# Performance work log

Hardware: AMD Instinct MI355X
Metric: run time of the kernel (lower is better)

Reference implementation:

```python
import jax, jax.numpy as jnp
import numpy as np

N_NODES = 10000


def gcn_conv(x, W, b, src, dst, num_nodes):
    # PyG GCNConv (eval): h = x @ W; add self-loops; symmetric norm D^-1/2 A D^-1/2; sum-aggregate; + bias
    h = x @ W  # [N, out]
    loop = jnp.arange(num_nodes, dtype=src.dtype)
    s = jnp.concatenate([src, loop])  # [E+N]
    d = jnp.concatenate([dst, loop])
    deg = jax.ops.segment_sum(jnp.ones_like(d, dtype=h.dtype), d, num_segments=num_nodes)
    dinv = jnp.where(deg > 0, jax.lax.rsqrt(deg), 0.0)
    norm = dinv[s] * dinv[d]  # [E+N]
    msg = h[s] * norm[:, None]  # gather + scale
    out = jax.ops.segment_sum(msg, d, num_segments=num_nodes)  # scatter-add to dst
    return out + b


def setup_inputs() -> dict:
    key = jax.random.key(0)
    k1, k2, k3, k4 = jax.random.split(key, 4)
    in_c, hid_c, out_c = 512, 512, 256
    x = jax.random.normal(k1, (N_NODES, in_c), dtype=jnp.float32)
    edge_index = jax.random.randint(k2, (2, 160000), 0, N_NODES, dtype=jnp.int64)
    W1 = jax.random.normal(k3, (in_c, hid_c), dtype=jnp.float32) * (1.0 / np.sqrt(in_c))
    b1 = jnp.zeros((hid_c,), dtype=jnp.float32)
    W2 = jax.random.normal(k4, (hid_c, out_c), dtype=jnp.float32) * (1.0 / np.sqrt(hid_c))
    b2 = jnp.zeros((out_c,), dtype=jnp.float32)
    return {"x": x, "edge_index": edge_index, "W1": W1, "b1": b1, "W2": W2, "b2": b2}


def reference(x, edge_index, W1, b1, W2, b2):
    src, dst = edge_index[0], edge_index[1]
    h = gcn_conv(x, W1, b1, src, dst, N_NODES)
    h = jax.nn.relu(h)
    # dropout(p=0.5) is identity in eval mode
    z = gcn_conv(h, W2, b2, src, dst, N_NODES)
    return z
```

## Files before the change

### kernel.cpp

```cpp
#include <hip/hip_runtime.h>

#define NN   10000

typedef float f32x4 __attribute__((ext_vector_type(4)));
typedef short s16x8 __attribute__((ext_vector_type(8)));
typedef short s16x4 __attribute__((ext_vector_type(4)));

__device__ __forceinline__ unsigned int f2bf(float f) {
  unsigned int u = __float_as_uint(f);
  return (u + 0x7fffu + ((u >> 16) & 1u)) >> 16;
}
__device__ __forceinline__ float bf2f(unsigned int h) {
  return __uint_as_float(h << 16);
}

__global__ void k_zero_int(int* __restrict__ p, int n) {
  int i = blockIdx.x * blockDim.x + threadIdx.x;
  if (i < n) p[i] = 0;
}

__global__ void k_count(const int* __restrict__ dst, int E, int* __restrict__ cnt) {
  int i = blockIdx.x * blockDim.x + threadIdx.x;
  if (i < E) atomicAdd(&cnt[dst[i]], 1);
}

__global__ __launch_bounds__(256) void k_scan(const int* __restrict__ cnt, int n,
                                              int* __restrict__ offs, float* __restrict__ dinv) {
  __shared__ int part[256];
  int t = threadIdx.x;
  int chunk = (n + 255) / 256;
  int lo = t * chunk, hi = min(lo + chunk, n);
  int s = 0;
  for (int i = lo; i < hi; ++i) s += cnt[i];
  part[t] = s;
  __syncthreads();
  for (int d = 1; d < 256; d <<= 1) {
    int v = (t >= d) ? part[t - d] : 0;
    __syncthreads();
    part[t] += v;
    __syncthreads();
  }
  int run = (t == 0) ? 0 : part[t - 1];
  for (int i = lo; i < hi; ++i) {
    offs[i] = run;
    int c = cnt[i];
    run += c;
    dinv[i] = rsqrtf((float)(c + 1));
  }
  if (t == 255) offs[n] = run;
}

__global__ void k_fill(const int* __restrict__ src, const int* __restrict__ dst, int E,
                       const int* __restrict__ offs, int* __restrict__ cur, int* __restrict__ csr) {
  int i = blockIdx.x * blockDim.x + threadIdx.x;
  if (i < E) {
    int d = dst[i];
    int p = atomicAdd(&cur[d], 1);
    csr[offs[d] + p] = src[i];
  }
}

__global__ void k_convw(const float* __restrict__ W, unsigned short* __restrict__ WT, int N) {
  int i = blockIdx.x * blockDim.x + threadIdx.x;
  if (i >= 512 * N) return;
  int k = i / N, n = i - k * N;
  float f = W[i];
  unsigned int hb = f2bf(f);
  WT[(size_t)n * 1024 + k] = (unsigned short)hb;
  WT[(size_t)n * 1024 + 512 + k] = (unsigned short)f2bf(f - bf2f(hb));
}

__global__ __launch_bounds__(256) void k_gemm_mfma(
    const float* __restrict__ A, const unsigned short* __restrict__ WT,
    float* __restrict__ C, int M, int N, int NTN) {
  __shared__ short Wh[64 * 40], Wl[64 * 40], Ahs[64 * 40], Als[64 * 40];

  int nwg = gridDim.x;
  int q = nwg >> 3, r = nwg & 7;
  int xcd = blockIdx.x & 7, idx = blockIdx.x >> 3;
  int swz = (xcd < r ? xcd * (q + 1) : r * (q + 1) + (xcd - r) * q) + idx;
  int bn = (swz % NTN) * 64;
  int bm = (swz / NTN) * 64;

  int t = threadIdx.x;
  int wid = t >> 6, lane = t & 63;
  int wn = wid & 1, wm = wid >> 1;
  int lr = lane & 15, lg = lane >> 4;

  int wrow = t >> 2, kg8 = (t & 3) * 8;
  int arow = t >> 3, kc4 = (t & 7) * 4;

  f32x4 acc[2][2];
  #pragma unroll
  for (int i = 0; i < 2; ++i)
    #pragma unroll
    for (int j = 0; j < 2; ++j) acc[i][j] = (f32x4){0.f, 0.f, 0.f, 0.f};

  const unsigned short* wbase = WT + (size_t)(bn + wrow) * 1024;

  for (int kk = 0; kk < 512; kk += 32) {
    __syncthreads();
    *(s16x8*)&Wh[wrow * 40 + kg8] = *(const s16x8*)&wbase[kk + kg8];
    *(s16x8*)&Wl[wrow * 40 + kg8] = *(const s16x8*)&wbase[512 + kk + kg8];
    #pragma unroll
    for (int p = 0; p < 2; ++p) {
      int row = arow + p * 32;
      int grow = bm + row;
      float4 v = make_float4(0.f, 0.f, 0.f, 0.f);
      if (grow < M) v = *(const float4*)&A[(size_t)grow * 512 + kk + kc4];
      float fs[4] = {v.x, v.y, v.z, v.w};
      s16x4 hv, lv;
      #pragma unroll
      for (int j = 0; j < 4; ++j) {
        unsigned int hb = f2bf(fs[j]);
        hv[j] = (short)hb;
        lv[j] = (short)f2bf(fs[j] - bf2f(hb));
      }
      *(s16x4*)&Ahs[row * 40 + kc4] = hv;
      *(s16x4*)&Als[row * 40 + kc4] = lv;
    }
    __syncthreads();

    s16x8 fwh[2], fwl[2], fah[2], fal[2];
    #pragma unroll
    for (int i = 0; i < 2; ++i) {
      int nr = wn * 32 + i * 16 + lr;
      int mr = wm * 32 + i * 16 + lr;
      fwh[i] = *(const s16x8*)&Wh[nr * 40 + lg * 8];
      fwl[i] = *(const s16x8*)&Wl[nr * 40 + lg * 8];
      fah[i] = *(const s16x8*)&Ahs[mr * 40 + lg * 8];
      fal[i] = *(const s16x8*)&Als[mr * 40 + lg * 8];
    }
    #pragma unroll
    for (int mi = 0; mi < 2; ++mi)
      #pragma unroll
      for (int ni = 0; ni < 2; ++ni) {
        acc[mi][ni] = __builtin_amdgcn_mfma_f32_16x16x32_bf16(fwh[ni], fah[mi], acc[mi][ni], 0, 0, 0);
        acc[mi][ni] = __builtin_amdgcn_mfma_f32_16x16x32_bf16(fwl[ni], fah[mi], acc[mi][ni], 0, 0, 0);
        acc[mi][ni] = __builtin_amdgcn_mfma_f32_16x16x32_bf16(fwh[ni], fal[mi], acc[mi][ni], 0, 0, 0);
      }
  }

  #pragma unroll
  for (int mi = 0; mi < 2; ++mi) {
    int m = bm + wm * 32 + mi * 16 + lr;
    if (m < M) {
      #pragma unroll
      for (int ni = 0; ni < 2; ++ni) {
        int n0 = bn + wn * 32 + ni * 16 + lg * 4;
        *(f32x4*)&C[(size_t)m * N + n0] = acc[mi][ni];
      }
    }
  }
}

template <int F, bool RELU>
__global__ __launch_bounds__(256) void k_agg(const float* __restrict__ H, const float* __restrict__ dinv,
                                             const int* __restrict__ offs, const int* __restrict__ csr,
                                             const float* __restrict__ bias, float* __restrict__ out) {
  constexpr int FT = F / 4;
  constexpr int EG = 256 / FT;
  __shared__ float red[256][4];
  int node = blockIdx.x;
  int t = threadIdx.x;
  int fc = t % FT;
  int eg = t / FT;
  int lo = offs[node], hi = offs[node + 1];
  float ax = 0.f, ay = 0.f, az = 0.f, aw = 0.f;
  for (int j = lo + eg; j < hi; j += EG) {
    int s = csr[j];
    float w = dinv[s];
    const float4 v = *(const float4*)&H[(size_t)s * F + fc * 4];
    ax += w * v.x; ay += w * v.y; az += w * v.z; aw += w * v.w;
  }
  red[t][0] = ax; red[t][1] = ay; red[t][2] = az; red[t][3] = aw;
  __syncthreads();
  if (eg == 0) {
    #pragma unroll
    for (int g = 1; g < EG; ++g) {
      ax += red[g * FT + fc][0];
      ay += red[g * FT + fc][1];
      az += red[g * FT + fc][2];
      aw += red[g * FT + fc][3];
    }
    float wd = dinv[node];
    const float4 sv = *(const float4*)&H[(size_t)node * F + fc * 4];
    float ox = wd * (ax + wd * sv.x) + bias[fc * 4 + 0];
    float oy = wd * (ay + wd * sv.y) + bias[fc * 4 + 1];
    float oz = wd * (az + wd * sv.z) + bias[fc * 4 + 2];
    float ow = wd * (aw + wd * sv.w) + bias[fc * 4 + 3];
    if (RELU) {
      ox = fmaxf(ox, 0.f); oy = fmaxf(oy, 0.f); oz = fmaxf(oz, 0.f); ow = fmaxf(ow, 0.f);
    }
    *(float4*)&out[(size_t)node * F + fc * 4] = make_float4(ox, oy, oz, ow);
  }
}

extern "C" void kernel_launch(void* const* d_in, const int* in_sizes, int n_in,
                              void* d_out, int out_size, void* d_ws, size_t ws_size,
                              hipStream_t stream) {
  (void)n_in; (void)out_size; (void)ws_size;
  const float* x  = (const float*)d_in[0];
  const int*   ei = (const int*)d_in[1];
  const float* W1 = (const float*)d_in[2];
  const float* b1 = (const float*)d_in[3];
  const float* W2 = (const float*)d_in[4];
  const float* b2 = (const float*)d_in[5];
  float* out = (float*)d_out;

  int E = in_sizes[1] / 2;
  const int* src = ei;
  const int* dst = ei + E;

  char* w = (char*)d_ws;
  float*          dinv = (float*)(w);
  int*            cnt  = (int*)(w + 65536);
  int*            cur  = (int*)(w + 131072);
  int*            offs = (int*)(w + 196608);
  int*            csr  = (int*)(w + 262144);
  unsigned short* WT1  = (unsigned short*)(w + 1048576);
  unsigned short* WT2  = (unsigned short*)(w + 2097152);
  float*          h1   = (float*)(w + 3145728);
  float*          a1   = (float*)(w + 23625728ULL);
  float*          h2   = h1;

  k_zero_int<<<(NN + 255) / 256, 256, 0, stream>>>(cnt, NN);
  k_zero_int<<<(NN + 255) / 256, 256, 0, stream>>>(cur, NN);
  k_count<<<(E + 255) / 256, 256, 0, stream>>>(dst, E, cnt);
  k_scan<<<1, 256, 0, stream>>>(cnt, NN, offs, dinv);
  k_fill<<<(E + 255) / 256, 256, 0, stream>>>(src, dst, E, offs, cur, csr);

  k_convw<<<(512 * 512 + 255) / 256, 256, 0, stream>>>(W1, WT1, 512);
  k_convw<<<(512 * 256 + 255) / 256, 256, 0, stream>>>(W2, WT2, 256);

  int ntm = (NN + 63) / 64;
  k_gemm_mfma<<<8 * ntm, 256, 0, stream>>>(x, WT1, h1, NN, 512, 8);
  k_agg<512, true><<<NN, 256, 0, stream>>>(h1, dinv, offs, csr, b1, a1);
  k_gemm_mfma<<<4 * ntm, 256, 0, stream>>>(a1, WT2, h2, NN, 256, 4);
  k_agg<256, false><<<NN, 256, 0, stream>>>(h2, dinv, offs, csr, b2, out);
}
```

Measured before the change: 258.1 us.

## Store GEMM outputs and hidden activations in bf16 to halve gather traffic

Both GEMMs now write bf16 instead of fp32, and the aggregation kernels gather bf16 rows, 8 features per thread with fp32 accumulation. The first aggregation writes its ReLU output as bf16, so the second GEMM reads bf16 directly and drops the low-part split and its extra MFMA. This halves memory traffic in the bandwidth-bound edge gathers and the intermediate writes. In exchange the hidden features lose precision, which may push results outside tolerance.

```diff
diff --git a/kernel.cpp b/kernel.cpp
--- a/kernel.cpp
+++ b/kernel.cpp
@@ -70,10 +70,12 @@
   WT[(size_t)n * 1024 + 512 + k] = (unsigned short)f2bf(f - bf2f(hb));
 }
 
+template <bool ASPLIT>
 __global__ __launch_bounds__(256) void k_gemm_mfma(
-    const float* __restrict__ A, const unsigned short* __restrict__ WT,
-    float* __restrict__ C, int M, int N, int NTN) {
-  __shared__ short Wh[64 * 40], Wl[64 * 40], Ahs[64 * 40], Als[64 * 40];
+    const void* __restrict__ Ap, const unsigned short* __restrict__ WT,
+    unsigned short* __restrict__ C, int M, int N, int NTN) {
+  __shared__ short Wh[64 * 40], Wl[64 * 40], Ahs[64 * 40];
+  __shared__ short Als[ASPLIT ? 64 * 40 : 8];
 
   int nwg = gridDim.x;
   int q = nwg >> 3, r = nwg & 7;
@@ -89,6 +91,7 @@
 
   int wrow = t >> 2, kg8 = (t & 3) * 8;
   int arow = t >> 3, kc4 = (t & 7) * 4;
+  int brow = t >> 2, kb8 = (t & 3) * 8;
 
   f32x4 acc[2][2];
   #pragma unroll
@@ -102,22 +105,31 @@
     __syncthreads();
     *(s16x8*)&Wh[wrow * 40 + kg8] = *(const s16x8*)&wbase[kk + kg8];
     *(s16x8*)&Wl[wrow * 40 + kg8] = *(const s16x8*)&wbase[512 + kk + kg8];
-    #pragma unroll
-    for (int p = 0; p < 2; ++p) {
-      int row = arow + p * 32;
-      int grow = bm + row;
-      float4 v = make_float4(0.f, 0.f, 0.f, 0.f);
-      if (grow < M) v = *(const float4*)&A[(size_t)grow * 512 + kk + kc4];
-      float fs[4] = {v.x, v.y, v.z, v.w};
-      s16x4 hv, lv;
-      #pragma unroll
-      for (int j = 0; j < 4; ++j) {
-        unsigned int hb = f2bf(fs[j]);
-        hv[j] = (short)hb;
-        lv[j] = (short)f2bf(fs[j] - bf2f(hb));
+    if (ASPLIT) {
+      const float* A = (const float*)Ap;
+      #pragma unroll
+      for (int p = 0; p < 2; ++p) {
+        int row = arow + p * 32;
+        int grow = bm + row;
+        float4 v = make_float4(0.f, 0.f, 0.f, 0.f);
+        if (grow < M) v = *(const float4*)&A[(size_t)grow * 512 + kk + kc4];
+        float fs[4] = {v.x, v.y, v.z, v.w};
+        s16x4 hv, lv;
+        #pragma unroll
+        for (int j = 0; j < 4; ++j) {
+          unsigned int hb = f2bf(fs[j]);
+          hv[j] = (short)hb;
+          lv[j] = (short)f2bf(fs[j] - bf2f(hb));
+        }
+        *(s16x4*)&Ahs[row * 40 + kc4] = hv;
+        *(s16x4*)&Als[row * 40 + kc4] = lv;
       }
-      *(s16x4*)&Ahs[row * 40 + kc4] = hv;
-      *(s16x4*)&Als[row * 40 + kc4] = lv;
+    } else {
+      const unsigned short* Ab = (const unsigned short*)Ap;
+      int grow = bm + brow;
+      s16x8 v = (s16x8){0, 0, 0, 0, 0, 0, 0, 0};
+      if (grow < M) v = *(const s16x8*)&Ab[(size_t)grow * 512 + kk + kb8];
+      *(s16x8*)&Ahs[brow * 40 + kb8] = v;
     }
     __syncthreads();
 
@@ -129,7 +141,7 @@
       fwh[i] = *(const s16x8*)&Wh[nr * 40 + lg * 8];
       fwl[i] = *(const s16x8*)&Wl[nr * 40 + lg * 8];
       fah[i] = *(const s16x8*)&Ahs[mr * 40 + lg * 8];
-      fal[i] = *(const s16x8*)&Als[mr * 40 + lg * 8];
+      if (ASPLIT) fal[i] = *(const s16x8*)&Als[mr * 40 + lg * 8];
     }
     #pragma unroll
     for (int mi = 0; mi < 2; ++mi)
@@ -137,7 +149,8 @@
       for (int ni = 0; ni < 2; ++ni) {
         acc[mi][ni] = __builtin_amdgcn_mfma_f32_16x16x32_bf16(fwh[ni], fah[mi], acc[mi][ni], 0, 0, 0);
         acc[mi][ni] = __builtin_amdgcn_mfma_f32_16x16x32_bf16(fwl[ni], fah[mi], acc[mi][ni], 0, 0, 0);
-        acc[mi][ni] = __builtin_amdgcn_mfma_f32_16x16x32_bf16(fwh[ni], fal[mi], acc[mi][ni], 0, 0, 0);
+        if (ASPLIT)
+          acc[mi][ni] = __builtin_amdgcn_mfma_f32_16x16x32_bf16(fwh[ni], fal[mi], acc[mi][ni], 0, 0, 0);
       }
   }
 
@@ -148,51 +161,66 @@
       #pragma unroll
       for (int ni = 0; ni < 2; ++ni) {
         int n0 = bn + wn * 32 + ni * 16 + lg * 4;
-        *(f32x4*)&C[(size_t)m * N + n0] = acc[mi][ni];
+        ushort4 cv;
+        cv.x = (unsigned short)f2bf(acc[mi][ni][0]);
+        cv.y = (unsigned short)f2bf(acc[mi][ni][1]);
+        cv.z = (unsigned short)f2bf(acc[mi][ni][2]);
+        cv.w = (unsigned short)f2bf(acc[mi][ni][3]);
+        *(ushort4*)&C[(size_t)m * N + n0] = cv;
       }
     }
   }
 }
 
-template <int F, bool RELU>
-__global__ __launch_bounds__(256) void k_agg(const float* __restrict__ H, const float* __restrict__ dinv,
-                                             const int* __restrict__ offs, const int* __restrict__ csr,
-                                             const float* __restrict__ bias, float* __restrict__ out) {
-  constexpr int FT = F / 4;
+template <int F, bool RELU, bool OUTBF16>
+__global__ __launch_bounds__(256) void k_agg_bf(
+    const unsigned short* __restrict__ H, const float* __restrict__ dinv,
+    const int* __restrict__ offs, const int* __restrict__ csr,
+    const float* __restrict__ bias, void* __restrict__ outp) {
+  constexpr int FT = F / 8;
   constexpr int EG = 256 / FT;
-  __shared__ float red[256][4];
+  __shared__ float red[256][8];
   int node = blockIdx.x;
   int t = threadIdx.x;
   int fc = t % FT;
   int eg = t / FT;
   int lo = offs[node], hi = offs[node + 1];
-  float ax = 0.f, ay = 0.f, az = 0.f, aw = 0.f;
-  for (int j = lo + eg; j < hi; j += EG) {
-    int s = csr[j];
+  float a[8];
+  #pragma unroll
+  for (int j = 0; j < 8; ++j) a[j] = 0.f;
+  for (int e = lo + eg; e < hi; e += EG) {
+    int s = csr[e];
     float w = dinv[s];
-    const float4 v = *(const float4*)&H[(size_t)s * F + fc * 4];
-    ax += w * v.x; ay += w * v.y; az += w * v.z; aw += w * v.w;
-  }
-  red[t][0] = ax; red[t][1] = ay; red[t][2] = az; red[t][3] = aw;
+    s16x8 v = *(const s16x8*)&H[(size_t)s * F + fc * 8];
+    #pragma unroll
+    for (int j = 0; j < 8; ++j) a[j] += w * bf2f((unsigned short)v[j]);
+  }
+  #pragma unroll
+  for (int j = 0; j < 8; ++j) red[t][j] = a[j];
   __syncthreads();
   if (eg == 0) {
     #pragma unroll
-    for (int g = 1; g < EG; ++g) {
-      ax += red[g * FT + fc][0];
-      ay += red[g * FT + fc][1];
-      az += red[g * FT + fc][2];
-      aw += red[g * FT + fc][3];
-    }
+    for (int g = 1; g < EG; ++g)
+      #pragma unroll
+      for (int j = 0; j < 8; ++j) a[j] += red[g * FT + fc][j];
     float wd = dinv[node];
-    const float4 sv = *(const float4*)&H[(size_t)node * F + fc * 4];
-    float ox = wd * (ax + wd * sv.x) + bias[fc * 4 + 0];
-    float oy = wd * (ay + wd * sv.y) + bias[fc * 4 + 1];
-    float oz = wd * (az + wd * sv.z) + bias[fc * 4 + 2];
-    float ow = wd * (aw + wd * sv.w) + bias[fc * 4 + 3];
-    if (RELU) {
-      ox = fmaxf(ox, 0.f); oy = fmaxf(oy, 0.f); oz = fmaxf(oz, 0.f); ow = fmaxf(ow, 0.f);
-    }
-    *(float4*)&out[(size_t)node * F + fc * 4] = make_float4(ox, oy, oz, ow);
+    s16x8 sv = *(const s16x8*)&H[(size_t)node * F + fc * 8];
+    float o[8];
+    #pragma unroll
+    for (int j = 0; j < 8; ++j) {
+      o[j] = wd * (a[j] + wd * bf2f((unsigned short)sv[j])) + bias[fc * 8 + j];
+      if (RELU) o[j] = fmaxf(o[j], 0.f);
+    }
+    if (OUTBF16) {
+      s16x8 hv;
+      #pragma unroll
+      for (int j = 0; j < 8; ++j) hv[j] = (short)f2bf(o[j]);
+      *(s16x8*)&((unsigned short*)outp)[(size_t)node * F + fc * 8] = hv;
+    } else {
+      float* op = (float*)outp;
+      *(float4*)&op[(size_t)node * F + fc * 8]     = make_float4(o[0], o[1], o[2], o[3]);
+      *(float4*)&op[(size_t)node * F + fc * 8 + 4] = make_float4(o[4], o[5], o[6], o[7]);
+    }
   }
 }
 
@@ -220,9 +248,9 @@
   int*            csr  = (int*)(w + 262144);
   unsigned short* WT1  = (unsigned short*)(w + 1048576);
   unsigned short* WT2  = (unsigned short*)(w + 2097152);
-  float*          h1   = (float*)(w + 3145728);
-  float*          a1   = (float*)(w + 23625728ULL);
-  float*          h2   = h1;
+  unsigned short* h1   = (unsigned short*)(w + 3145728);
+  unsigned short* a1   = (unsigned short*)(w + 14680064);
+  unsigned short* h2   = (unsigned short*)(w + 26214400);
 
   k_zero_int<<<(NN + 255) / 256, 256, 0, stream>>>(cnt, NN);
   k_zero_int<<<(NN + 255) / 256, 256, 0, stream>>>(cur, NN);
@@ -234,8 +262,8 @@
   k_convw<<<(512 * 256 + 255) / 256, 256, 0, stream>>>(W2, WT2, 256);
 
   int ntm = (NN + 63) / 64;
-  k_gemm_mfma<<<8 * ntm, 256, 0, stream>>>(x, WT1, h1, NN, 512, 8);
-  k_agg<512, true><<<NN, 256, 0, stream>>>(h1, dinv, offs, csr, b1, a1);
-  k_gemm_mfma<<<4 * ntm, 256, 0, stream>>>(a1, WT2, h2, NN, 256, 4);
-  k_agg<256, false><<<NN, 256, 0, stream>>>(h2, dinv, offs, csr, b2, out);
-}
+  k_gemm_mfma<true><<<8 * ntm, 256, 0, stream>>>(x, WT1, h1, NN, 512, 8);
+  k_agg_bf<512, true, true><<<NN, 256, 0, stream>>>(h1, dinv, offs, csr, b1, a1);
+  k_gemm_mfma<false><<<4 * ntm, 256, 0, stream>>>(a1, WT2, h2, NN, 256, 4);
+  k_agg_bf<256, false, false><<<NN, 256, 0, stream>>>(h2, dinv, offs, csr, b2, out);
+}
```

Measured after the change: 219.4 us. 15.0% less time.
